# Kernel optimization log

Hardware: AMD Instinct MI355X
Metric: run time of the kernel (lower is better)

The kernel has to match this reference:

```python
import jax, jax.numpy as jnp
import numpy as np

EMBED = 768
HIDDEN = 3072
HEADS = 12
EPS = 1e-6


def _ln(x, g, b):
    mu = jnp.mean(x, axis=-1, keepdims=True)
    var = jnp.mean(jnp.square(x - mu), axis=-1, keepdims=True)
    return (x - mu) / jnp.sqrt(var + EPS) * g + b


def setup_inputs() -> dict:
    key = jax.random.key(0)
    ks = jax.random.split(key, 12)
    s = lambda fan_in: 1.0 / np.sqrt(fan_in)
    x = jax.random.normal(ks[0], (16, 1024, EMBED), dtype=jnp.float32)
    return {
        "x": x,
        "ln1_g": jnp.ones((EMBED,), jnp.float32),
        "ln1_b": jnp.zeros((EMBED,), jnp.float32),
        "qkv_w": jax.random.uniform(ks[1], (3 * EMBED, EMBED), jnp.float32, -s(EMBED), s(EMBED)),
        "qkv_b": jax.random.uniform(ks[2], (3 * EMBED,), jnp.float32, -s(EMBED), s(EMBED)),
        "proj_w": jax.random.uniform(ks[3], (EMBED, EMBED), jnp.float32, -s(EMBED), s(EMBED)),
        "proj_b": jax.random.uniform(ks[4], (EMBED,), jnp.float32, -s(EMBED), s(EMBED)),
        "ln2_g": jnp.ones((EMBED,), jnp.float32),
        "ln2_b": jnp.zeros((EMBED,), jnp.float32),
        "fc1_w": jax.random.uniform(ks[5], (HIDDEN, EMBED), jnp.float32, -s(EMBED), s(EMBED)),
        "fc1_b": jax.random.uniform(ks[6], (HIDDEN,), jnp.float32, -s(EMBED), s(EMBED)),
        "fc2_w": jax.random.uniform(ks[7], (EMBED, HIDDEN), jnp.float32, -s(HIDDEN), s(HIDDEN)),
        "fc2_b": jax.random.uniform(ks[8], (EMBED,), jnp.float32, -s(HIDDEN), s(HIDDEN)),
    }


def reference(x, ln1_g, ln1_b, qkv_w, qkv_b, proj_w, proj_b, ln2_g, ln2_b, fc1_w, fc1_b, fc2_w, fc2_b):
    B, N, D = x.shape
    Hd = D // HEADS
    scale = Hd ** -0.5
    # attention branch
    xn = _ln(x, ln1_g, ln1_b)
    qkv = xn @ qkv_w.T + qkv_b  # [B,N,3D]
    qkv = qkv.reshape(B, N, 3, HEADS, Hd).transpose(2, 0, 3, 1, 4)
    q, k, v = qkv[0], qkv[1], qkv[2]  # [B,H,N,Hd]
    attn = jax.nn.softmax(jnp.einsum("bhqd,bhkd->bhqk", q, k) * scale, axis=-1)
    ctx = jnp.einsum("bhqk,bhkd->bhqd", attn, v)
    ctx = ctx.transpose(0, 2, 1, 3).reshape(B, N, D)
    x = x + ctx @ proj_w.T + proj_b
    # MLP branch
    h = _ln(x, ln2_g, ln2_b)
    h = jax.nn.gelu(h @ fc1_w.T + fc1_b, approximate=False)
    x = x + h @ fc2_w.T + fc2_b
    return x
```

## Files before the change

### kernel.cpp

```cpp
#include <hip/hip_runtime.h>
#include <math.h>


typedef unsigned short u16;
typedef __attribute__((ext_vector_type(8))) short bf16x8;
typedef __attribute__((ext_vector_type(4))) float f32x4;

#define MFMA_BF16(a, b, c) __builtin_amdgcn_mfma_f32_16x16x32_bf16((a), (b), (c), 0, 0, 0)
#define MEMFENCE asm volatile("" ::: "memory")
#define WAITV(N) asm volatile("s_waitcnt vmcnt(" #N ")" ::: "memory")
#define WAITLGKM0 asm volatile("s_waitcnt lgkmcnt(0)" ::: "memory")
#define SCHED0 __builtin_amdgcn_sched_barrier(0)
#define EXP2F(x) __builtin_amdgcn_exp2f(x)

#define QSCALE 0.18033688011112042f
#define C8LOG2E 11.541560327111707f

__device__ __forceinline__ float bf2f(u16 v) {
    return __uint_as_float(((unsigned)v) << 16);
}
__device__ __forceinline__ u16 f2bf(float f) {
    unsigned u = __float_as_uint(f);
    u += 0x7fffu + ((u >> 16) & 1u);
    return (u16)(u >> 16);
}
__device__ __forceinline__ unsigned cvtpk_bf16(float lo, float hi) {
    unsigned r;
    asm volatile("v_cvt_pk_bf16_f32 %0, %1, %2" : "=v"(r) : "v"(lo), "v"(hi));
    return r;
}

__device__ __forceinline__ float gelu_fast(float v) {
    const float t = v * v;
    const float z = v * (1.5957691216f + 0.0713548162f * t);
    const float e = __expf(-z);
    return v * __builtin_amdgcn_rcpf(1.0f + e);
}

typedef __attribute__((address_space(1))) const void gvoid;
typedef __attribute__((address_space(3))) void lvoid;
__device__ __forceinline__ void gll16(const void* g, void* l) {
    __builtin_amdgcn_global_load_lds((gvoid*)g, (lvoid*)l, 16, 0, 0);
}

__global__ __launch_bounds__(256) void cast32(const float* __restrict__ src,
                                              u16* __restrict__ dst, int n8) {
    const int i = blockIdx.x * 256 + threadIdx.x;
    if (i >= n8) return;
    const float4 a = ((const float4*)src)[2 * i];
    const float4 b = ((const float4*)src)[2 * i + 1];
    bf16x8 r;
    r[0] = (short)f2bf(a.x); r[1] = (short)f2bf(a.y);
    r[2] = (short)f2bf(a.z); r[3] = (short)f2bf(a.w);
    r[4] = (short)f2bf(b.x); r[5] = (short)f2bf(b.y);
    r[6] = (short)f2bf(b.z); r[7] = (short)f2bf(b.w);
    ((bf16x8*)dst)[i] = r;
}

__global__ __launch_bounds__(256) void ln_kernel(const float* __restrict__ x,
                                                 const float* __restrict__ g,
                                                 const float* __restrict__ b,
                                                 u16* __restrict__ out) {
    const int row = blockIdx.x;
    const int t = threadIdx.x;
    const float* xr = x + (size_t)row * 768;
    float v0 = xr[t], v1 = xr[t + 256], v2 = xr[t + 512];
    float s = v0 + v1 + v2;
    float sq = v0 * v0 + v1 * v1 + v2 * v2;
#pragma unroll
    for (int off = 32; off > 0; off >>= 1) {
        s += __shfl_down(s, off);
        sq += __shfl_down(sq, off);
    }
    __shared__ float red_s[4], red_sq[4], sh_mu, sh_rs;
    const int wave = t >> 6, lane = t & 63;
    if (lane == 0) { red_s[wave] = s; red_sq[wave] = sq; }
    __syncthreads();
    if (t == 0) {
        float S = red_s[0] + red_s[1] + red_s[2] + red_s[3];
        float SQ = red_sq[0] + red_sq[1] + red_sq[2] + red_sq[3];
        float mu = S * (1.0f / 768.0f);
        float var = SQ * (1.0f / 768.0f) - mu * mu;
        sh_mu = mu;
        sh_rs = 1.0f / sqrtf(fmaxf(var, 0.0f) + 1e-6f);
    }
    __syncthreads();
    const float mu = sh_mu, rs = sh_rs;
    u16* orow = out + (size_t)row * 768;
    orow[t]       = f2bf((v0 - mu) * rs * g[t]       + b[t]);
    orow[t + 256] = f2bf((v1 - mu) * rs * g[t + 256] + b[t + 256]);
    orow[t + 512] = f2bf((v2 - mu) * rs * g[t + 512] + b[t + 512]);
}

template <int EPI, int BF16B>
__global__ __launch_bounds__(256, 2) void gemm2(
        const u16* __restrict__ A, const void* __restrict__ Bv,
        const float* __restrict__ bias, const float* __restrict__ res,
        void* __restrict__ Cv, u16* __restrict__ vtb, int N, int K) {
    __shared__ __align__(16) u16 As[128 * 32];
    __shared__ __align__(16) u16 Bs[128 * 32];
    const int t = threadIdx.x;
    const int wave = t >> 6, lane = t & 63;
    const int quad = lane >> 4, mr = lane & 15;
    const int wm = wave >> 1, wn = wave & 1;
    const int m0 = blockIdx.y * 128;
    const int n0 = blockIdx.x * 128;

    f32x4 acc[4][4];
#pragma unroll
    for (int i = 0; i < 4; i++)
#pragma unroll
        for (int j = 0; j < 4; j++) acc[i][j] = (f32x4){0.f, 0.f, 0.f, 0.f};

    const int seg = wave * 2;
    const int drow = lane >> 2;
    const int dcol = (lane & 3) * 8;
    const int sr = t >> 2, skv = t & 3;

    for (int k0 = 0; k0 < K; k0 += 32) {
#pragma unroll
        for (int c = 0; c < 2; c++) {
            const int rowA = (seg + c) * 16 + drow;
            gll16(A + (size_t)(m0 + rowA) * K + k0 + dcol, &As[(seg + c) * 512]);
        }
        if (BF16B) {
            const u16* Bh = (const u16*)Bv;
#pragma unroll
            for (int c = 0; c < 2; c++) {
                const int rowB = (seg + c) * 16 + drow;
                gll16(Bh + (size_t)(n0 + rowB) * K + k0 + dcol, &Bs[(seg + c) * 512]);
            }
        } else {
            const float* Bf = (const float*)Bv;
#pragma unroll
            for (int half = 0; half < 2; half++) {
                const float* src = Bf + (size_t)(n0 + sr + half * 64) * K + k0 + skv * 8;
                const float4 a = *(const float4*)src;
                const float4 b2 = *(const float4*)(src + 4);
                bf16x8 r;
                r[0] = (short)f2bf(a.x);  r[1] = (short)f2bf(a.y);
                r[2] = (short)f2bf(a.z);  r[3] = (short)f2bf(a.w);
                r[4] = (short)f2bf(b2.x); r[5] = (short)f2bf(b2.y);
                r[6] = (short)f2bf(b2.z); r[7] = (short)f2bf(b2.w);
                *(bf16x8*)&Bs[(sr + half * 64) * 32 + skv * 8] = r;
            }
        }
        __syncthreads();
        bf16x8 af[4], bfr[4];
#pragma unroll
        for (int i = 0; i < 4; i++)
            af[i] = *(const bf16x8*)&As[(wm * 64 + i * 16 + mr) * 32 + quad * 8];
#pragma unroll
        for (int j = 0; j < 4; j++)
            bfr[j] = *(const bf16x8*)&Bs[(wn * 64 + j * 16 + mr) * 32 + quad * 8];
#pragma unroll
        for (int i = 0; i < 4; i++)
#pragma unroll
            for (int j = 0; j < 4; j++)
                acc[i][j] = MFMA_BF16(af[i], bfr[j], acc[i][j]);
        __syncthreads();
    }

#pragma unroll
    for (int i = 0; i < 4; i++) {
#pragma unroll
        for (int r = 0; r < 4; r++) {
            const int m = m0 + wm * 64 + i * 16 + quad * 4 + r;
#pragma unroll
            for (int j = 0; j < 4; j++) {
                const int n = n0 + wn * 64 + j * 16 + mr;
                float v = acc[i][j][r] + bias[n];
                if (EPI == 1) {
                    v = gelu_fast(v);
                    ((u16*)Cv)[(size_t)m * N + n] = f2bf(v);
                } else if (EPI == 2) {
                    v += res[(size_t)m * N + n];
                    ((float*)Cv)[(size_t)m * N + n] = v;
                } else {
                    if (n < 1536) {
                        const float vq = (n < 768) ? v * QSCALE : v;
                        ((u16*)Cv)[(size_t)m * 1536 + n] = f2bf(vq);
                    } else {
                        const int h = (n - 1536) >> 6, hd = (n - 1536) & 63;
                        const int bb = m >> 10, pos = m & 1023;
                        vtb[((size_t)(bb * 12 + h) * 64 + hd) * 1024 + pos] = f2bf(v);
                    }
                }
            }
        }
    }
}

#define AFRAG(T, ROW, KS) \
    (*(const bf16x8*)&(T)[(ROW)][(((((KS) << 2) | quad)) ^ ((ROW) & 7)) << 3])

#define ACCUM(ACCEL, AF, BF)                                  \
    do {                                                      \
        if (EPI == 3) (ACCEL) = MFMA_BF16((AF), (BF), (ACCEL)); \
        else          (ACCEL) = MFMA_BF16((BF), (AF), (ACCEL)); \
    } while (0)

template <int EPI>
__global__ __launch_bounds__(512, 2) void gemm8(
        const u16* __restrict__ A, const u16* __restrict__ Bw,
        const float* __restrict__ bias, const float* __restrict__ res,
        void* __restrict__ Cv, u16* __restrict__ vtb, int N, int K) {
    __shared__ __align__(16) u16 SMEM[4][256][64];
    u16(&As)[2][256][64] = *reinterpret_cast<u16(*)[2][256][64]>(&SMEM[0][0][0]);
    u16(&Bs)[2][256][64] = *reinterpret_cast<u16(*)[2][256][64]>(&SMEM[2][0][0]);
    const int t = threadIdx.x;
    const int wave = t >> 6, lane = t & 63;
    const int quad = lane >> 4, mr = lane & 15;
    const int wm = wave >> 2, wn = wave & 3;
    const int gx = gridDim.x;
    const int nwg = gx * gridDim.y;
    int bid = blockIdx.y * gx + blockIdx.x;
    bid = (bid & 7) * (nwg >> 3) + (bid >> 3);
    const int m0 = (bid / gx) * 256, n0 = (bid % gx) * 256;
    const int NT = K >> 6;

    const int srow = wave * 8 + (lane >> 3);
    const int sgrp = ((lane & 7) ^ (lane >> 3)) * 8;

    const u16* Abase = A + (size_t)(m0 + srow) * K + sgrp;
    const u16* Bbase = Bw + (size_t)(n0 + srow) * K + sgrp;

#define STAGE_A(BI, SLOT, KT) \
    gll16(Abase + ((size_t)(SLOT) * 64) * K + (KT) * 64, &As[BI][(SLOT) * 64 + wave * 8][0])
#define STAGE_B(BI, SLOT, KT) \
    gll16(Bbase + ((size_t)(SLOT) * 64) * K + (KT) * 64, &Bs[BI][(SLOT) * 64 + wave * 8][0])

    STAGE_A(0, 0, 0); STAGE_A(0, 2, 0);
    STAGE_B(0, 0, 0); STAGE_B(0, 1, 0);
    STAGE_B(0, 2, 0); STAGE_B(0, 3, 0);
    STAGE_A(0, 1, 0); STAGE_A(0, 3, 0);
    if (NT > 1) { STAGE_A(1, 0, 1); STAGE_A(1, 2, 1); STAGE_B(1, 0, 1); STAGE_B(1, 1, 1); }

    f32x4 acc[8][4];
#pragma unroll
    for (int i = 0; i < 8; i++)
#pragma unroll
        for (int j = 0; j < 4; j++) acc[i][j] = (f32x4){0.f, 0.f, 0.f, 0.f};

    if (NT > 1) { WAITV(6); } else { WAITV(2); }
    __builtin_amdgcn_s_barrier();
    SCHED0;

    for (int kt = 0; kt < NT; ++kt) {
        const int bi = kt & 1;
        const u16(*Ab)[64] = As[bi];
        const u16(*Bb)[64] = Bs[bi];
        const bool st1 = (kt + 1 < NT);
        const bool st2 = (kt + 2 < NT);
        bf16x8 af[4], bfv[4];

#pragma unroll
        for (int i = 0; i < 4; i++) af[i] = AFRAG(Ab, wm * 128 + i * 16 + mr, 0);
#pragma unroll
        for (int j = 0; j < 4; j++) bfv[j] = AFRAG(Bb, wn * 64 + j * 16 + mr, 0);
        if (st1) { STAGE_B(bi ^ 1, 2, kt + 1); STAGE_B(bi ^ 1, 3, kt + 1); }
        SCHED0;
        __builtin_amdgcn_s_barrier();
        WAITLGKM0;
        SCHED0;
        __builtin_amdgcn_s_setprio(1);
#pragma unroll
        for (int i = 0; i < 4; i++)
#pragma unroll
            for (int j = 0; j < 4; j++)
                ACCUM(acc[i][j], af[i], bfv[j]);
        __builtin_amdgcn_s_setprio(0);
        SCHED0;
        if (st1) { WAITV(6); } else { WAITV(0); }
        __builtin_amdgcn_s_barrier();
        SCHED0;

#pragma unroll
        for (int i = 0; i < 4; i++) af[i] = AFRAG(Ab, wm * 128 + 64 + i * 16 + mr, 0);
        if (st1) { STAGE_A(bi ^ 1, 1, kt + 1); STAGE_A(bi ^ 1, 3, kt + 1); }
        SCHED0;
        __builtin_amdgcn_s_barrier();
        WAITLGKM0;
        SCHED0;
        __builtin_amdgcn_s_setprio(1);
#pragma unroll
        for (int i = 0; i < 4; i++)
#pragma unroll
            for (int j = 0; j < 4; j++)
                ACCUM(acc[4 + i][j], af[i], bfv[j]);
        __builtin_amdgcn_s_setprio(0);
        SCHED0;
        __builtin_amdgcn_s_barrier();
        SCHED0;

#pragma unroll
        for (int i = 0; i < 4; i++) af[i] = AFRAG(Ab, wm * 128 + i * 16 + mr, 1);
#pragma unroll
        for (int j = 0; j < 4; j++) bfv[j] = AFRAG(Bb, wn * 64 + j * 16 + mr, 1);
        SCHED0;
        __builtin_amdgcn_s_barrier();
        WAITLGKM0;
        SCHED0;
        __builtin_amdgcn_s_setprio(1);
#pragma unroll
        for (int i = 0; i < 4; i++)
#pragma unroll
            for (int j = 0; j < 4; j++)
                ACCUM(acc[i][j], af[i], bfv[j]);
        __builtin_amdgcn_s_setprio(0);
        SCHED0;
        __builtin_amdgcn_s_barrier();
        SCHED0;

#pragma unroll
        for (int i = 0; i < 4; i++) af[i] = AFRAG(Ab, wm * 128 + 64 + i * 16 + mr, 1);
        if (st2) { STAGE_A(bi, 0, kt + 2); STAGE_A(bi, 2, kt + 2);
                   STAGE_B(bi, 0, kt + 2); STAGE_B(bi, 1, kt + 2); }
        SCHED0;
        __builtin_amdgcn_s_barrier();
        WAITLGKM0;
        SCHED0;
        __builtin_amdgcn_s_setprio(1);
#pragma unroll
        for (int i = 0; i < 4; i++)
#pragma unroll
            for (int j = 0; j < 4; j++)
                ACCUM(acc[4 + i][j], af[i], bfv[j]);
        __builtin_amdgcn_s_setprio(0);
        SCHED0;
        if (st2) { WAITV(6); } else if (st1) { WAITV(2); }
        __builtin_amdgcn_s_barrier();
        SCHED0;
    }

    if (EPI == 3) {
        if (n0 >= 1536) {
            u16* Ls = &SMEM[0][0][0];
            __syncthreads();
#pragma unroll
            for (int i = 0; i < 8; i++) {
                const int mbase = wm * 128 + i * 16 + quad * 4;
                const int mch = mbase >> 3, mlo = mbase & 7;
#pragma unroll
                for (int j = 0; j < 4; j++) {
                    const int nl = wn * 64 + j * 16 + mr;
                    float v0 = acc[i][j][0] + bias[n0 + nl];
                    float v1 = acc[i][j][1] + bias[n0 + nl];
                    float v2 = acc[i][j][2] + bias[n0 + nl];
                    float v3 = acc[i][j][3] + bias[n0 + nl];
                    ushort4 w;
                    w.x = f2bf(v0); w.y = f2bf(v1); w.z = f2bf(v2); w.w = f2bf(v3);
                    *(ushort4*)(Ls + nl * 256 + ((mch ^ (nl & 7)) << 3) + mlo) = w;
                }
            }
            __syncthreads();
            const int bb = m0 >> 10, pos0 = m0 & 1023;
#pragma unroll
            for (int it = 0; it < 32; it++) {
                const int nl = it * 8 + wave;
                const int h = (n0 - 1536 + nl) >> 6;
                const int hd = nl & 63;
                const int mch = (lane >> 1) ^ (nl & 7);
                const ushort4 v =
                    *(const ushort4*)(Ls + nl * 256 + (mch << 3) + (lane & 1) * 4);
                u16* dst = vtb + ((size_t)(bb * 12 + h) * 64 + hd) * 1024 + pos0 + lane * 4;
                *(ushort4*)dst = v;
            }
        } else {
#pragma unroll
            for (int i = 0; i < 8; i++) {
#pragma unroll
                for (int r = 0; r < 4; r++) {
                    const int m = m0 + wm * 128 + (i >> 2) * 64 + (i & 3) * 16 + quad * 4 + r;
#pragma unroll
                    for (int j = 0; j < 4; j++) {
                        const int n = n0 + wn * 64 + j * 16 + mr;
                        float v = acc[i][j][r] + bias[n];
                        const float vq = (n < 768) ? v * QSCALE : v;
                        ((u16*)Cv)[(size_t)m * 1536 + n] = f2bf(vq);
                    }
                }
            }
        }
    } else {
#pragma unroll
        for (int ii = 0; ii < 8; ii++) {
            const int m = m0 + wm * 128 + (ii >> 2) * 64 + (ii & 3) * 16 + mr;
#pragma unroll
            for (int j = 0; j < 4; j++) {
                const int n = n0 + wn * 64 + j * 16 + quad * 4;
                const float4 b4 = *(const float4*)&bias[n];
                const float v0 = acc[ii][j][0] + b4.x;
                const float v1 = acc[ii][j][1] + b4.y;
                const float v2 = acc[ii][j][2] + b4.z;
                const float v3 = acc[ii][j][3] + b4.w;
                if (EPI == 1) {
                    ushort4 w;
                    w.x = f2bf(gelu_fast(v0)); w.y = f2bf(gelu_fast(v1));
                    w.z = f2bf(gelu_fast(v2)); w.w = f2bf(gelu_fast(v3));
                    *(ushort4*)&((u16*)Cv)[(size_t)m * N + n] = w;
                } else {
                    const float4 r4 = *(const float4*)&res[(size_t)m * N + n];
                    float4 o;
                    o.x = v0 + r4.x; o.y = v1 + r4.y; o.z = v2 + r4.z; o.w = v3 + r4.w;
                    *(float4*)&((float*)Cv)[(size_t)m * N + n] = o;
                }
            }
        }
    }
#undef STAGE_A
#undef STAGE_B
}

__global__ __launch_bounds__(256) void attn2(const u16* __restrict__ qkkb,
                                             const u16* __restrict__ vtb,
                                             u16* __restrict__ ctx) {
    __shared__ __align__(16) u16 Ks[2][64][72];
    __shared__ __align__(16) u16 Vt[2][64][72];
    __shared__ __align__(16) u16 Ps[64][72];
    const int L = blockIdx.y * gridDim.x + blockIdx.x;
    const int lxcd = L & 7, li = L >> 3;
    const int bh = lxcd * 24 + (li >> 4);
    const int q0 = (li & 15) * 64;
    const int b = bh / 12, h = bh % 12;
    const int t = threadIdx.x;
    const int wave = t >> 6, lane = t & 63, quad = lane >> 4, mr = lane & 15;

    const u16* qrow = qkkb + (size_t)(b * 1024 + q0 + wave * 16 + mr) * 1536 + h * 64;
    const bf16x8 qf0 = *(const bf16x8*)(qrow + quad * 8);
    const bf16x8 qf1 = *(const bf16x8*)(qrow + 32 + quad * 8);

    const u16* kbase = qkkb + (size_t)b * 1024 * 1536 + 768 + h * 64;
    const u16* vbase = vtb + (size_t)bh * 64 * 1024;

    const int srow = t >> 3;
    const int sv = t & 7;

    f32x4 oacc[4];
#pragma unroll
    for (int j = 0; j < 4; j++) oacc[j] = (f32x4){0.f, 0.f, 0.f, 0.f};
    float lsum = 0.f;

    bf16x8 pk0, pk1, pv0, pv1;
    pk0 = *(const bf16x8*)(kbase + (size_t)(srow)      * 1536 + sv * 8);
    pk1 = *(const bf16x8*)(kbase + (size_t)(srow + 32) * 1536 + sv * 8);
    pv0 = *(const bf16x8*)(vbase + (size_t)(srow)      * 1024 + sv * 8);
    pv1 = *(const bf16x8*)(vbase + (size_t)(srow + 32) * 1024 + sv * 8);
    *(bf16x8*)&Ks[0][srow][sv * 8] = pk0;
    *(bf16x8*)&Ks[0][srow + 32][sv * 8] = pk1;
    *(bf16x8*)&Vt[0][srow][sv * 8] = pv0;
    *(bf16x8*)&Vt[0][srow + 32][sv * 8] = pv1;

    for (int kt = 0; kt < 16; ++kt) {
        __syncthreads();
        const int cur = kt & 1;
        if (kt < 15) {
            const size_t ko = (size_t)(kt + 1) * 64;
            pk0 = *(const bf16x8*)(kbase + (ko + srow)      * 1536 + sv * 8);
            pk1 = *(const bf16x8*)(kbase + (ko + srow + 32) * 1536 + sv * 8);
            pv0 = *(const bf16x8*)(vbase + (size_t)(srow)      * 1024 + ko + sv * 8);
            pv1 = *(const bf16x8*)(vbase + (size_t)(srow + 32) * 1024 + ko + sv * 8);
        }
        f32x4 sf[4];
#pragma unroll
        for (int j = 0; j < 4; j++) {
            const bf16x8 kf0 = *(const bf16x8*)&Ks[cur][j * 16 + mr][quad * 8];
            const bf16x8 kf1 = *(const bf16x8*)&Ks[cur][j * 16 + mr][32 + quad * 8];
            f32x4 s = (f32x4){0.f, 0.f, 0.f, 0.f};
            s = MFMA_BF16(kf0, qf0, s);
            s = MFMA_BF16(kf1, qf1, s);
            sf[j] = s;
        }
#pragma unroll
        for (int j = 0; j < 4; j++) {
            const float p0 = EXP2F(sf[j][0] - C8LOG2E);
            const float p1 = EXP2F(sf[j][1] - C8LOG2E);
            const float p2 = EXP2F(sf[j][2] - C8LOG2E);
            const float p3 = EXP2F(sf[j][3] - C8LOG2E);
            lsum += (p0 + p1) + (p2 + p3);
            uint2 w;
            w.x = cvtpk_bf16(p0, p1);
            w.y = cvtpk_bf16(p2, p3);
            *(uint2*)&Ps[wave * 16 + mr][j * 16 + quad * 4] = w;
        }
        __asm__ __volatile__("s_waitcnt lgkmcnt(0)" ::: "memory");
#pragma unroll
        for (int st = 0; st < 2; st++) {
            const bf16x8 pf = *(const bf16x8*)&Ps[wave * 16 + mr][st * 32 + quad * 8];
#pragma unroll
            for (int j = 0; j < 4; j++) {
                const bf16x8 vf = *(const bf16x8*)&Vt[cur][j * 16 + mr][st * 32 + quad * 8];
                oacc[j] = MFMA_BF16(vf, pf, oacc[j]);
            }
        }
        if (kt < 15) {
            const int nxt = cur ^ 1;
            *(bf16x8*)&Ks[nxt][srow][sv * 8] = pk0;
            *(bf16x8*)&Ks[nxt][srow + 32][sv * 8] = pk1;
            *(bf16x8*)&Vt[nxt][srow][sv * 8] = pv0;
            *(bf16x8*)&Vt[nxt][srow + 32][sv * 8] = pv1;
        }
    }

    lsum += __shfl_xor(lsum, 16);
    lsum += __shfl_xor(lsum, 32);
    const float inv = 1.0f / lsum;
    u16* dst = ctx + (size_t)(b * 1024 + q0 + wave * 16 + mr) * 768 + h * 64;
#pragma unroll
    for (int j = 0; j < 4; j++) {
        ushort4 w;
        w.x = f2bf(oacc[j][0] * inv);
        w.y = f2bf(oacc[j][1] * inv);
        w.z = f2bf(oacc[j][2] * inv);
        w.w = f2bf(oacc[j][3] * inv);
        *(ushort4*)(dst + j * 16 + quad * 4) = w;
    }
}

extern "C" void kernel_launch(void* const* d_in, const int* in_sizes, int n_in,
                              void* d_out, int out_size, void* d_ws, size_t ws_size,
                              hipStream_t stream) {
    const float* x      = (const float*)d_in[0];
    const float* ln1_g  = (const float*)d_in[1];
    const float* ln1_b  = (const float*)d_in[2];
    const float* qkv_w  = (const float*)d_in[3];
    const float* qkv_b  = (const float*)d_in[4];
    const float* proj_w = (const float*)d_in[5];
    const float* proj_b = (const float*)d_in[6];
    const float* ln2_g  = (const float*)d_in[7];
    const float* ln2_b  = (const float*)d_in[8];
    const float* fc1_w  = (const float*)d_in[9];
    const float* fc1_b  = (const float*)d_in[10];
    const float* fc2_w  = (const float*)d_in[11];
    const float* fc2_b  = (const float*)d_in[12];
    float* out = (float*)d_out;

    char* base = (char*)d_ws + 1024;
    u16* xn   = (u16*)base;
    u16* qkkb = (u16*)(base + 25165824);
    u16* vtb  = (u16*)(base + 75497472);
    u16* h1   = (u16*)(base + 25165824);
    u16* ctxb = xn;
    u16* hn   = xn;

    const size_t WOFF = 125830144ull;
    const bool big = ws_size >= 139985920ull;
    u16* wqkv  = (u16*)((char*)d_ws + WOFF);
    u16* wproj = (u16*)((char*)d_ws + WOFF + 3538944);
    u16* wfc1  = (u16*)((char*)d_ws + WOFF + 4718592);
    u16* wfc2  = (u16*)((char*)d_ws + WOFF + 9437184);

    if (big) {
        cast32<<<dim3(864),  dim3(256), 0, stream>>>(qkv_w,  wqkv,  221184);
        cast32<<<dim3(288),  dim3(256), 0, stream>>>(proj_w, wproj, 73728);
        cast32<<<dim3(1152), dim3(256), 0, stream>>>(fc1_w,  wfc1,  294912);
        cast32<<<dim3(1152), dim3(256), 0, stream>>>(fc2_w,  wfc2,  294912);
    }

    ln_kernel<<<dim3(16384), dim3(256), 0, stream>>>(x, ln1_g, ln1_b, xn);

    if (big)
        gemm8<3><<<dim3(9, 64), dim3(512), 0, stream>>>(
            xn, wqkv, qkv_b, nullptr, qkkb, vtb, 2304, 768);
    else
        gemm2<3, 0><<<dim3(18, 128), dim3(256), 0, stream>>>(
            xn, qkv_w, qkv_b, nullptr, qkkb, vtb, 2304, 768);

    attn2<<<dim3(16, 192), dim3(256), 0, stream>>>(qkkb, vtb, ctxb);

    if (big)
        gemm8<2><<<dim3(3, 64), dim3(512), 0, stream>>>(
            ctxb, wproj, proj_b, x, out, nullptr, 768, 768);
    else
        gemm2<2, 0><<<dim3(6, 128), dim3(256), 0, stream>>>(
            ctxb, proj_w, proj_b, x, out, nullptr, 768, 768);

    ln_kernel<<<dim3(16384), dim3(256), 0, stream>>>(out, ln2_g, ln2_b, hn);

    if (big)
        gemm8<1><<<dim3(12, 64), dim3(512), 0, stream>>>(
            hn, wfc1, fc1_b, nullptr, h1, nullptr, 3072, 768);
    else
        gemm2<1, 0><<<dim3(24, 128), dim3(256), 0, stream>>>(
            hn, fc1_w, fc1_b, nullptr, h1, nullptr, 3072, 768);

    if (big)
        gemm8<2><<<dim3(3, 64), dim3(512), 0, stream>>>(
            h1, wfc2, fc2_b, out, out, nullptr, 768, 3072);
    else
        gemm2<2, 0><<<dim3(6, 128), dim3(256), 0, stream>>>(
            h1, fc2_w, fc2_b, out, out, nullptr, 768, 3072);
}
```

Before: 582.5 us.

## Collapse GEMM main loop into one barrier per K-tile with bulk prefetch

Replaces the four-phase K-loop in the 256x256 bf16 MFMA GEMM with a simpler schedule. All next-tile global-to-LDS loads are issued at the start of each iteration, and all fragment loads and MFMAs run back-to-back, with one LDS wait and one barrier per tile. The prologue now loads the first tile in A-then-B order with adjusted vmcnt waits. This removes most intra-tile barriers and the s_setprio toggling to cut synchronisation overhead. The cost is losing the hand-interleaved overlap between LDS reads, global loads and MFMA work, which leaves more of the scheduling to the compiler.

```diff
diff --git a/kernel.cpp b/kernel.cpp
--- a/kernel.cpp
+++ b/kernel.cpp
@@ -230,10 +230,8 @@
 #define STAGE_B(BI, SLOT, KT) \
     gll16(Bbase + ((size_t)(SLOT) * 64) * K + (KT) * 64, &Bs[BI][(SLOT) * 64 + wave * 8][0])
 
-    STAGE_A(0, 0, 0); STAGE_A(0, 2, 0);
-    STAGE_B(0, 0, 0); STAGE_B(0, 1, 0);
-    STAGE_B(0, 2, 0); STAGE_B(0, 3, 0);
-    STAGE_A(0, 1, 0); STAGE_A(0, 3, 0);
+    STAGE_A(0, 0, 0); STAGE_A(0, 1, 0); STAGE_A(0, 2, 0); STAGE_A(0, 3, 0);
+    STAGE_B(0, 0, 0); STAGE_B(0, 1, 0); STAGE_B(0, 2, 0); STAGE_B(0, 3, 0);
     if (NT > 1) { STAGE_A(1, 0, 1); STAGE_A(1, 2, 1); STAGE_B(1, 0, 1); STAGE_B(1, 1, 1); }
 
     f32x4 acc[8][4];
@@ -242,7 +240,7 @@
 #pragma unroll
         for (int j = 0; j < 4; j++) acc[i][j] = (f32x4){0.f, 0.f, 0.f, 0.f};
 
-    if (NT > 1) { WAITV(6); } else { WAITV(2); }
+    if (NT > 1) { WAITV(4); } else { WAITV(0); }
     __builtin_amdgcn_s_barrier();
     SCHED0;
 
@@ -252,83 +250,48 @@
         const u16(*Bb)[64] = Bs[bi];
         const bool st1 = (kt + 1 < NT);
         const bool st2 = (kt + 2 < NT);
+
+        if (st1) { STAGE_B(bi ^ 1, 2, kt + 1); STAGE_B(bi ^ 1, 3, kt + 1);
+                   STAGE_A(bi ^ 1, 1, kt + 1); STAGE_A(bi ^ 1, 3, kt + 1); }
+
         bf16x8 af[4], bfv[4];
-
+#pragma unroll
+        for (int j = 0; j < 4; j++) bfv[j] = AFRAG(Bb, wn * 64 + j * 16 + mr, 0);
 #pragma unroll
         for (int i = 0; i < 4; i++) af[i] = AFRAG(Ab, wm * 128 + i * 16 + mr, 0);
 #pragma unroll
-        for (int j = 0; j < 4; j++) bfv[j] = AFRAG(Bb, wn * 64 + j * 16 + mr, 0);
-        if (st1) { STAGE_B(bi ^ 1, 2, kt + 1); STAGE_B(bi ^ 1, 3, kt + 1); }
-        SCHED0;
-        __builtin_amdgcn_s_barrier();
+        for (int i = 0; i < 4; i++)
+#pragma unroll
+            for (int j = 0; j < 4; j++) ACCUM(acc[i][j], af[i], bfv[j]);
+#pragma unroll
+        for (int i = 0; i < 4; i++) af[i] = AFRAG(Ab, wm * 128 + 64 + i * 16 + mr, 0);
+#pragma unroll
+        for (int i = 0; i < 4; i++)
+#pragma unroll
+            for (int j = 0; j < 4; j++) ACCUM(acc[4 + i][j], af[i], bfv[j]);
+#pragma unroll
+        for (int j = 0; j < 4; j++) bfv[j] = AFRAG(Bb, wn * 64 + j * 16 + mr, 1);
+#pragma unroll
+        for (int i = 0; i < 4; i++) af[i] = AFRAG(Ab, wm * 128 + i * 16 + mr, 1);
+#pragma unroll
+        for (int i = 0; i < 4; i++)
+#pragma unroll
+            for (int j = 0; j < 4; j++) ACCUM(acc[i][j], af[i], bfv[j]);
+#pragma unroll
+        for (int i = 0; i < 4; i++) af[i] = AFRAG(Ab, wm * 128 + 64 + i * 16 + mr, 1);
+#pragma unroll
+        for (int i = 0; i < 4; i++)
+#pragma unroll
+            for (int j = 0; j < 4; j++) ACCUM(acc[4 + i][j], af[i], bfv[j]);
+
         WAITLGKM0;
-        SCHED0;
-        __builtin_amdgcn_s_setprio(1);
-#pragma unroll
-        for (int i = 0; i < 4; i++)
-#pragma unroll
-            for (int j = 0; j < 4; j++)
-                ACCUM(acc[i][j], af[i], bfv[j]);
-        __builtin_amdgcn_s_setprio(0);
-        SCHED0;
-        if (st1) { WAITV(6); } else { WAITV(0); }
-        __builtin_amdgcn_s_barrier();
-        SCHED0;
-
-#pragma unroll
-        for (int i = 0; i < 4; i++) af[i] = AFRAG(Ab, wm * 128 + 64 + i * 16 + mr, 0);
-        if (st1) { STAGE_A(bi ^ 1, 1, kt + 1); STAGE_A(bi ^ 1, 3, kt + 1); }
-        SCHED0;
-        __builtin_amdgcn_s_barrier();
-        WAITLGKM0;
-        SCHED0;
-        __builtin_amdgcn_s_setprio(1);
-#pragma unroll
-        for (int i = 0; i < 4; i++)
-#pragma unroll
-            for (int j = 0; j < 4; j++)
-                ACCUM(acc[4 + i][j], af[i], bfv[j]);
-        __builtin_amdgcn_s_setprio(0);
         SCHED0;
         __builtin_amdgcn_s_barrier();
         SCHED0;
-
-#pragma unroll
-        for (int i = 0; i < 4; i++) af[i] = AFRAG(Ab, wm * 128 + i * 16 + mr, 1);
-#pragma unroll
-        for (int j = 0; j < 4; j++) bfv[j] = AFRAG(Bb, wn * 64 + j * 16 + mr, 1);
-        SCHED0;
-        __builtin_amdgcn_s_barrier();
-        WAITLGKM0;
-        SCHED0;
-        __builtin_amdgcn_s_setprio(1);
-#pragma unroll
-        for (int i = 0; i < 4; i++)
-#pragma unroll
-            for (int j = 0; j < 4; j++)
-                ACCUM(acc[i][j], af[i], bfv[j]);
-        __builtin_amdgcn_s_setprio(0);
-        SCHED0;
-        __builtin_amdgcn_s_barrier();
-        SCHED0;
-
-#pragma unroll
-        for (int i = 0; i < 4; i++) af[i] = AFRAG(Ab, wm * 128 + 64 + i * 16 + mr, 1);
         if (st2) { STAGE_A(bi, 0, kt + 2); STAGE_A(bi, 2, kt + 2);
                    STAGE_B(bi, 0, kt + 2); STAGE_B(bi, 1, kt + 2); }
         SCHED0;
-        __builtin_amdgcn_s_barrier();
-        WAITLGKM0;
-        SCHED0;
-        __builtin_amdgcn_s_setprio(1);
-#pragma unroll
-        for (int i = 0; i < 4; i++)
-#pragma unroll
-            for (int j = 0; j < 4; j++)
-                ACCUM(acc[4 + i][j], af[i], bfv[j]);
-        __builtin_amdgcn_s_setprio(0);
-        SCHED0;
-        if (st2) { WAITV(6); } else if (st1) { WAITV(2); }
+        if (st2) { WAITV(4); } else { WAITV(0); }
         __builtin_amdgcn_s_barrier();
         SCHED0;
     }
```

After: 563.8 us. 3.2% less time.
